# Kernel optimization log

Measured on AMD Instinct MI355X. Metric: run time of the kernel, lower is better.

The kernel has to match this reference:

```python
import jax, jax.numpy as jnp
import numpy as np

D_IN, D_OUT, N_EXP, D_HID = 1024, 1024, 8, 2048
N_TOK = 4096


def setup_inputs() -> dict:
    key = jax.random.key(0)
    ks = jax.random.split(key, 8)
    s_in = 1.0 / np.sqrt(D_IN)
    s_hid = 1.0 / np.sqrt(D_HID)
    s_out = 1.0 / np.sqrt(D_OUT)
    return {
        "x": jax.random.normal(ks[0], (N_TOK, D_IN), dtype=jnp.float32),
        # per-expert MLP weights, stacked along expert axis
        "W1": jax.random.uniform(ks[1], (N_EXP, D_IN, D_HID), jnp.float32, -s_in, s_in),
        "b1": jax.random.uniform(ks[2], (N_EXP, D_HID), jnp.float32, -s_in, s_in),
        "W2": jax.random.uniform(ks[3], (N_EXP, D_HID, D_OUT), jnp.float32, -s_hid, s_hid),
        "b2": jax.random.uniform(ks[4], (N_EXP, D_OUT), jnp.float32, -s_hid, s_hid),
        # shared final linear
        "Wf": jax.random.uniform(ks[5], (D_OUT, D_OUT), jnp.float32, -s_out, s_out),
        "bf": jax.random.uniform(ks[6], (D_OUT,), jnp.float32, -s_out, s_out),
    }


def reference(x, W1, b1, W2, b2, Wf, bf):
    # All experts applied to the same x: batched (grouped) GEMMs via einsum.
    h = jax.nn.relu(jnp.einsum("nd,edh->neh", x, W1) + b1[None])     # [N, E, H]
    y = jnp.einsum("neh,eho->neo", h, W2) + b2[None]                  # [N, E, O]
    z = jnp.einsum("neo,op->nep", y, Wf) + bf                         # shared final linear
    out = jnp.mean(z, axis=1)                                         # mean over experts
    return (out, 0)
```

## Files before the change

### kernel.cpp

```cpp
#include <hip/hip_runtime.h>
#include <hip/hip_bf16.h>


#define D_IN  1024
#define D_HID 2048
#define D_OUT 1024
#define N_EXP 8
#define N_TOK 4096

typedef __attribute__((ext_vector_type(4))) float  f32x4;
typedef __attribute__((ext_vector_type(8))) short  s16x8;
typedef __attribute__((ext_vector_type(4))) short  s16x4;
typedef __attribute__((ext_vector_type(8))) __bf16 b16x8;

static __device__ __forceinline__ f32x4 mfma16x16x32(s16x8 a, s16x8 b, f32x4 c) {
  return __builtin_amdgcn_mfma_f32_16x16x32_bf16(
      __builtin_bit_cast(b16x8, a), __builtin_bit_cast(b16x8, b), c, 0, 0, 0);
}

#define GLDS16(gptr, lptr)                                                         \
  __builtin_amdgcn_global_load_lds(                                               \
      (const __attribute__((address_space(1))) void*)(gptr),                      \
      (__attribute__((address_space(3))) void*)(lptr), 16, 0, 0)

#define WAITV(n) asm volatile("s_waitcnt vmcnt(" #n ")" ::: "memory")
#define SBAR()                                                                     \
  do {                                                                             \
    __builtin_amdgcn_sched_barrier(0);                                             \
    __builtin_amdgcn_s_barrier();                                                  \
    __builtin_amdgcn_sched_barrier(0);                                             \
  } while (0)

static __device__ __forceinline__ short f2b(float f) {
  return __builtin_bit_cast(short, __float2bfloat16(f));
}
static __device__ __forceinline__ float b2f(short s) {
  return __bfloat162float(__builtin_bit_cast(__hip_bfloat16, s));
}


__global__ void cast_x_kernel(const float* __restrict__ in, short* __restrict__ out, int n4) {
  int i = blockIdx.x * blockDim.x + threadIdx.x;
  if (i >= n4) return;
  f32x4 v = ((const f32x4*)in)[i];
  s16x4 o;
  o[0] = f2b(v[0]); o[1] = f2b(v[1]); o[2] = f2b(v[2]); o[3] = f2b(v[3]);
  ((s16x4*)out)[i] = o;
}

__global__ void tcast_kernel(const float* __restrict__ in, short* __restrict__ out, int R, int C) {
  __shared__ float t[32][33];
  size_t slab = (size_t)blockIdx.z * R * C;
  const float* src = in + slab;
  short* dst = out + slab;
  int c0 = blockIdx.x * 32, r0 = blockIdx.y * 32;
  int tx = threadIdx.x, ty = threadIdx.y;
#pragma unroll
  for (int i = 0; i < 32; i += 8)
    t[ty + i][tx] = src[(size_t)(r0 + ty + i) * C + c0 + tx];
  __syncthreads();
#pragma unroll
  for (int i = 0; i < 32; i += 8)
    dst[(size_t)(c0 + ty + i) * R + r0 + tx] = f2b(t[tx][ty + i]);
}

__global__ void b2mean_kernel(const float* __restrict__ b2, float* __restrict__ b2m) {
  int o = blockIdx.x * blockDim.x + threadIdx.x;
  if (o < D_OUT) {
    float s = 0.f;
#pragma unroll
    for (int e = 0; e < N_EXP; ++e) s += b2[e * D_OUT + o];
    b2m[o] = s * 0.125f;
  }
}


template <bool RELU>
__global__ __launch_bounds__(512, 2) void gemm256_p8_kernel(
    const short* __restrict__ A, const short* __restrict__ Bt,
    short* __restrict__ C, const float* __restrict__ bias,
    int K, int ldc, long sAe, long sBe, long sCe, long sBiasE) {
  extern __shared__ short lds[];
  const int tid = threadIdx.x, wid = tid >> 6, lane = tid & 63;
  const int e = blockIdx.z;
  const short* Ab = A + (size_t)e * sAe + (size_t)blockIdx.y * 256 * K;
  const short* Bb = Bt + (size_t)e * sBe + (size_t)blockIdx.x * 256 * K;

  const int strow = wid * 16 + (lane >> 2);
  const int stcol = ((lane & 3) ^ ((strow >> 1) & 3)) * 8;
  const int wm = wid >> 2, wn = wid & 3;
  const int lr = lane & 15;
  const int gp = ((lane >> 4) ^ ((lr >> 1) & 3)) * 8;

  f32x4 acc[8][4] = {};
  const int nkt = K / 64;
  const int niter = nkt / 2;

  auto SLOT = [&](int t, int ks, int ab) -> short* {
    return lds + (size_t)(t & 1) * 32768 + ab * 16384 + ks * 8192;
  };
  auto STAGE = [&](int t, int ks, int ab) {
    const short* src = ab ? Bb : Ab;
    short* dst = SLOT(t, ks, ab) + wid * 512;
    const size_t ko = (size_t)t * 64 + ks * 32 + stcol;
    GLDS16(src + (size_t)strow * K + ko, dst);
    GLDS16(src + (size_t)(128 + strow) * K + ko, dst + 4096);
  };
  auto LDA = [&](s16x8* av, int t, int h, int ks) {
    const short* s = SLOT(t, ks, 0);
#pragma unroll
    for (int m = 0; m < 4; ++m)
      av[m] = *(const s16x8*)&s[(wm * 128 + h * 64 + m * 16 + lr) * 32 + gp];
  };
  auto LDB = [&](s16x8* bv, int t, int ks) {
    const short* s = SLOT(t, ks, 1);
#pragma unroll
    for (int n = 0; n < 4; ++n)
      bv[n] = *(const s16x8*)&s[(wn * 64 + n * 16 + lr) * 32 + gp];
  };
  auto QUAD = [&](int h, const s16x8* av, const s16x8* bv) {
    __builtin_amdgcn_s_setprio(1);
#pragma unroll
    for (int m = 0; m < 4; ++m)
#pragma unroll
      for (int n = 0; n < 4; ++n)
        acc[h * 4 + m][n] = mfma16x16x32(av[m], bv[n], acc[h * 4 + m][n]);
    __builtin_amdgcn_s_setprio(0);
  };

  s16x8 av0[4], av1[4], bv0[4], bv1[4];

  STAGE(0, 0, 0); STAGE(0, 0, 1); STAGE(0, 1, 0); STAGE(0, 1, 1);
  STAGE(1, 0, 0); STAGE(1, 0, 1); STAGE(1, 1, 0);
  WAITV(10);
  SBAR();
  LDA(av1, 0, 0, 0);
  LDB(bv0, 0, 0);

  for (int i = 0; i < niter - 1; ++i) {
    const int t0 = 2 * i, t1 = t0 + 1;
     STAGE(t1, 1, 1); LDA(av0, t0, 1, 0);
           SBAR(); QUAD(0, av1, bv0);
     WAITV(8); STAGE(t0 + 2, 0, 0); LDA(av1, t0, 0, 1); LDB(bv1, t0, 1);
           SBAR(); QUAD(1, av0, bv0);
     STAGE(t0 + 2, 0, 1); LDA(av0, t0, 1, 1);
           SBAR(); QUAD(0, av1, bv1);
     WAITV(8); STAGE(t0 + 2, 1, 0); LDA(av1, t1, 0, 0); LDB(bv0, t1, 0);
           SBAR(); QUAD(1, av0, bv1);
     STAGE(t0 + 2, 1, 1); LDA(av0, t1, 1, 0);
           SBAR(); QUAD(0, av1, bv0);
     WAITV(8); STAGE(t0 + 3, 0, 0); LDA(av1, t1, 0, 1); LDB(bv1, t1, 1);
           SBAR(); QUAD(1, av0, bv0);
     STAGE(t0 + 3, 0, 1); LDA(av0, t1, 1, 1);
           SBAR(); QUAD(0, av1, bv1);
     WAITV(8); STAGE(t0 + 3, 1, 0); LDA(av1, t0 + 2, 0, 0); LDB(bv0, t0 + 2, 0);
           SBAR(); QUAD(1, av0, bv1);
  }
  {
    const int t0 = nkt - 2, t1 = nkt - 1;
     STAGE(t1, 1, 1); LDA(av0, t0, 1, 0);
           SBAR(); QUAD(0, av1, bv0);
     WAITV(8); LDA(av1, t0, 0, 1); LDB(bv1, t0, 1);
           SBAR(); QUAD(1, av0, bv0);
     LDA(av0, t0, 1, 1);
           SBAR(); QUAD(0, av1, bv1);
     WAITV(0); LDA(av1, t1, 0, 0); LDB(bv0, t1, 0);
           SBAR(); QUAD(1, av0, bv1);
     LDA(av0, t1, 1, 0);
           SBAR(); QUAD(0, av1, bv0);
     LDA(av1, t1, 0, 1); LDB(bv1, t1, 1);
           SBAR(); QUAD(1, av0, bv0);
     LDA(av0, t1, 1, 1);
           SBAR(); QUAD(0, av1, bv1);
     SBAR(); QUAD(1, av0, bv1);
  }

  __syncthreads();
  const int crow0 = wm * 128 + (lane >> 4) * 4;
  const int ccol0 = wn * 64 + lr;
#pragma unroll
  for (int ni = 0; ni < 4; ++ni) {
    const int col = ccol0 + ni * 16;
    const float bvv =
        bias ? bias[(size_t)e * sBiasE + (size_t)blockIdx.x * 256 + col] : 0.f;
#pragma unroll
    for (int mi = 0; mi < 8; ++mi)
#pragma unroll
      for (int j = 0; j < 4; ++j) {
        float v = acc[mi][ni][j] + bvv;
        if (RELU) v = v > 0.f ? v : 0.f;
        lds[(crow0 + mi * 16 + j) * 256 + col] = f2b(v);
      }
  }
  __syncthreads();
  short* Cp = C + (size_t)e * sCe + (size_t)blockIdx.y * 256 * ldc +
              (size_t)blockIdx.x * 256;
  const int cr = tid >> 5, cc = (tid & 31) * 8;
#pragma unroll
  for (int r = 0; r < 256; r += 16) {
    s16x8 v = *(const s16x8*)&lds[(r + cr) * 256 + cc];
    *(s16x8*)&Cp[(size_t)(r + cr) * ldc + cc] = v;
  }
}


template <bool RELU, bool OUTBF16>
__global__ __launch_bounds__(256) void gemm_bt_kernel(
    const short* __restrict__ A, const short* __restrict__ Bt, void* __restrict__ C,
    const float* __restrict__ bias, int K, int ldc,
    long sAe, long sBe, long sCe, long sBiasE) {
  constexpr int BM = 128, BN = 128, BK = 32;
  __shared__ short As[BM * BK];
  __shared__ short Bs[BN * BK];
  const int tid  = threadIdx.x;
  const int wid  = tid >> 6;
  const int lane = tid & 63;
  const int e    = blockIdx.z;

  const short* Ap = A + (size_t)e * sAe + (size_t)blockIdx.y * BM * K;
  const short* Bp = Bt + (size_t)e * sBe + (size_t)blockIdx.x * BN * K;

  const int srow = wid * 16 + (lane >> 2);
  const int scol = (lane & 3) * 8;
  const int wm = (wid >> 1) * 64, wn = (wid & 1) * 64;
  const int lr = lane & 15, lk = (lane >> 4) * 8;

  f32x4 acc[4][4] = {};
  const int nkt = K / BK;
  for (int kt = 0; kt < nkt; ++kt) {
    __syncthreads();
    const size_t ko = (size_t)kt * BK;
    GLDS16(Ap + (size_t)srow * K + ko + scol,        &As[wid * 512]);
    GLDS16(Ap + (size_t)(srow + 64) * K + ko + scol, &As[2048 + wid * 512]);
    GLDS16(Bp + (size_t)srow * K + ko + scol,        &Bs[wid * 512]);
    GLDS16(Bp + (size_t)(srow + 64) * K + ko + scol, &Bs[2048 + wid * 512]);
    __syncthreads();

    s16x8 a[4], b[4];
#pragma unroll
    for (int mi = 0; mi < 4; ++mi)
      a[mi] = *(const s16x8*)&As[(wm + mi * 16 + lr) * BK + lk];
#pragma unroll
    for (int ni = 0; ni < 4; ++ni)
      b[ni] = *(const s16x8*)&Bs[(wn + ni * 16 + lr) * BK + lk];
#pragma unroll
    for (int mi = 0; mi < 4; ++mi)
#pragma unroll
      for (int ni = 0; ni < 4; ++ni)
        acc[mi][ni] = mfma16x16x32(a[mi], b[ni], acc[mi][ni]);
  }

  const size_t Cbase = (size_t)e * sCe;
  const int row0 = blockIdx.y * BM + wm + (lane >> 4) * 4;
  const int col0 = blockIdx.x * BN + wn + lr;
#pragma unroll
  for (int ni = 0; ni < 4; ++ni) {
    const int col = col0 + ni * 16;
    const float bv = bias ? bias[(size_t)e * sBiasE + col] : 0.f;
#pragma unroll
    for (int mi = 0; mi < 4; ++mi) {
#pragma unroll
      for (int j = 0; j < 4; ++j) {
        float v = acc[mi][ni][j] + bv;
        if (RELU) v = v > 0.f ? v : 0.f;
        const size_t idx = Cbase + (size_t)(row0 + mi * 16 + j) * ldc + col;
        if (OUTBF16) ((short*)C)[idx] = f2b(v);
        else         ((float*)C)[idx] = v;
      }
    }
  }
}


__global__ void reduce_y_kernel(const short* __restrict__ yal, const float* __restrict__ b2m,
                                short* __restrict__ ybar, long slab, long total) {
  const size_t base = ((size_t)blockIdx.x * blockDim.x + threadIdx.x) * 8;
  if (base >= (size_t)total) return;
  float s[8] = {};
#pragma unroll
  for (int e = 0; e < N_EXP; ++e) {
    s16x8 v = *(const s16x8*)&yal[(size_t)e * slab + base];
#pragma unroll
    for (int j = 0; j < 8; ++j) s[j] += b2f(v[j]);
  }
  const int col = (int)(base & (D_OUT - 1));
  s16x8 o;
#pragma unroll
  for (int j = 0; j < 8; ++j) o[j] = f2b(s[j] * 0.125f + b2m[col + j]);
  *(s16x8*)&ybar[base] = o;
}

__global__ void tail_kernel(float* __restrict__ out, int from, int n) {
  int i = from + blockIdx.x * blockDim.x + threadIdx.x;
  if (i < n) out[i] = 0.f;
}


extern "C" void kernel_launch(void* const* d_in, const int* in_sizes, int n_in,
                              void* d_out, int out_size, void* d_ws, size_t ws_size,
                              hipStream_t stream) {
  const float* x  = (const float*)d_in[0];
  const float* W1 = (const float*)d_in[1];
  const float* b1 = (const float*)d_in[2];
  const float* W2 = (const float*)d_in[3];
  const float* b2 = (const float*)d_in[4];
  const float* Wf = (const float*)d_in[5];
  const float* bf = (const float*)d_in[6];
  float* out = (float*)d_out;

  const size_t sz_xb  = (size_t)N_TOK * D_IN * 2;
  const size_t sz_W1t = (size_t)N_EXP * D_HID * D_IN * 2;
  const size_t sz_W2t = (size_t)N_EXP * D_OUT * D_HID * 2;
  const size_t sz_Wft = (size_t)D_OUT * D_OUT * 2;
  const size_t sz_b2m = (size_t)D_OUT * 4;
  const size_t sz_ybr = (size_t)N_TOK * D_OUT * 2;
  const size_t fixed  = sz_xb + sz_W1t + sz_W2t + sz_Wft + sz_b2m + sz_ybr;
  const size_t per_full = (size_t)N_EXP * N_TOK * D_HID * 2
                        + (size_t)N_EXP * N_TOK * D_OUT * 2;
  int NC = 16;
  for (int c = 1; c <= 8; c <<= 1) {
    if (fixed + per_full / c <= ws_size) { NC = c; break; }
  }
  const int ntokc = N_TOK / NC;

  char* ws = (char*)d_ws;
  short* xb  = (short*)ws; ws += sz_xb;
  short* W1t = (short*)ws; ws += sz_W1t;
  short* W2t = (short*)ws; ws += sz_W2t;
  short* Wft = (short*)ws; ws += sz_Wft;
  float* b2m = (float*)ws; ws += sz_b2m;
  short* ybr = (short*)ws; ws += sz_ybr;
  short* h   = (short*)ws; ws += (size_t)N_EXP * ntokc * D_HID * 2;
  short* yal = (short*)ws;

  hipLaunchKernelGGL(cast_x_kernel, dim3(N_TOK * D_IN / 4 / 256), dim3(256), 0, stream,
                     x, xb, N_TOK * D_IN / 4);
  hipLaunchKernelGGL(tcast_kernel, dim3(D_HID / 32, D_IN / 32, N_EXP), dim3(32, 8), 0, stream,
                     W1, W1t, D_IN, D_HID);
  hipLaunchKernelGGL(tcast_kernel, dim3(D_OUT / 32, D_HID / 32, N_EXP), dim3(32, 8), 0, stream,
                     W2, W2t, D_HID, D_OUT);
  hipLaunchKernelGGL(tcast_kernel, dim3(D_OUT / 32, D_OUT / 32, 1), dim3(32, 8), 0, stream,
                     Wf, Wft, D_OUT, D_OUT);
  hipLaunchKernelGGL(b2mean_kernel, dim3(4), dim3(256), 0, stream, b2, b2m);

  const size_t ldsz = 131072;

  for (int c = 0; c < NC; ++c) {
    const short* xc = xb + (size_t)c * ntokc * D_IN;
    short* ybc = ybr + (size_t)c * ntokc * D_OUT;

    hipLaunchKernelGGL((gemm256_p8_kernel<true>),
                       dim3(D_HID / 256, ntokc / 256, N_EXP), dim3(512), ldsz, stream,
                       xc, W1t, h, b1, D_IN, D_HID,
                       0L, (long)D_HID * D_IN, (long)ntokc * D_HID, (long)D_HID);

    hipLaunchKernelGGL((gemm256_p8_kernel<false>),
                       dim3(D_OUT / 256, ntokc / 256, N_EXP), dim3(512), ldsz, stream,
                       h, W2t, yal, (const float*)nullptr, D_HID, D_OUT,
                       (long)ntokc * D_HID, (long)D_OUT * D_HID, (long)ntokc * D_OUT, 0L);

    hipLaunchKernelGGL(reduce_y_kernel, dim3(ntokc * D_OUT / 8 / 256), dim3(256), 0, stream,
                       yal, b2m, ybc, (long)ntokc * D_OUT, (long)ntokc * D_OUT);
  }

  hipLaunchKernelGGL((gemm_bt_kernel<false, false>),
                     dim3(D_OUT / 128, N_TOK / 128, 1), dim3(256), 0, stream,
                     ybr, Wft, d_out, bf, D_OUT, D_OUT, 0L, 0L, 0L, 0L);

  int tail = out_size - N_TOK * D_OUT;
  if (tail > 0)
    hipLaunchKernelGGL(tail_kernel, dim3((tail + 63) / 64), dim3(64), 0, stream,
                       out, N_TOK * D_OUT, out_size);
}
```

Measured before the change: 366.2 us.

## Restructure GEMM main loop to single-buffered register fragments with extra barriers

Rewrites the software-pipelined k-loop of the grouped GEMM kernel. Fragments are now loaded into a single register set right before use, gated by an explicit lgkmcnt(0) wait and an extra barrier per phase, instead of ping-ponging two fragment buffers so LDS reads overlap the previous MFMA quad. The global-to-LDS staging order and vmcnt thresholds are also changed. This frees registers, which may help occupancy, but it gives up LDS-read/MFMA overlap and doubles the barrier count.

```diff
diff --git a/kernel.cpp b/kernel.cpp
--- a/kernel.cpp
+++ b/kernel.cpp
@@ -28,6 +28,11 @@
   do {                                                                             \
     __builtin_amdgcn_sched_barrier(0);                                             \
     __builtin_amdgcn_s_barrier();                                                  \
+    __builtin_amdgcn_sched_barrier(0);                                             \
+  } while (0)
+#define LGKM0()                                                                    \
+  do {                                                                             \
+    asm volatile("s_waitcnt lgkmcnt(0)" ::: "memory");                             \
     __builtin_amdgcn_sched_barrier(0);                                             \
   } while (0)
 
@@ -128,51 +133,50 @@
     __builtin_amdgcn_s_setprio(0);
   };
 
-  s16x8 av0[4], av1[4], bv0[4], bv1[4];
-
-  STAGE(0, 0, 0); STAGE(0, 0, 1); STAGE(0, 1, 0); STAGE(0, 1, 1);
-  STAGE(1, 0, 0); STAGE(1, 0, 1); STAGE(1, 1, 0);
+  s16x8 av[4], bv[4];
+
+  STAGE(0, 0, 1); STAGE(0, 0, 0); STAGE(0, 1, 1); STAGE(0, 1, 0);
+  STAGE(1, 0, 1); STAGE(1, 0, 0); STAGE(1, 1, 1);
   WAITV(10);
   SBAR();
-  LDA(av1, 0, 0, 0);
-  LDB(bv0, 0, 0);
 
   for (int i = 0; i < niter - 1; ++i) {
-    const int t0 = 2 * i, t1 = t0 + 1;
-     STAGE(t1, 1, 1); LDA(av0, t0, 1, 0);
-           SBAR(); QUAD(0, av1, bv0);
-     WAITV(8); STAGE(t0 + 2, 0, 0); LDA(av1, t0, 0, 1); LDB(bv1, t0, 1);
-           SBAR(); QUAD(1, av0, bv0);
-     STAGE(t0 + 2, 0, 1); LDA(av0, t0, 1, 1);
-           SBAR(); QUAD(0, av1, bv1);
-     WAITV(8); STAGE(t0 + 2, 1, 0); LDA(av1, t1, 0, 0); LDB(bv0, t1, 0);
-           SBAR(); QUAD(1, av0, bv1);
-     STAGE(t0 + 2, 1, 1); LDA(av0, t1, 1, 0);
-           SBAR(); QUAD(0, av1, bv0);
-     WAITV(8); STAGE(t0 + 3, 0, 0); LDA(av1, t1, 0, 1); LDB(bv1, t1, 1);
-           SBAR(); QUAD(1, av0, bv0);
-     STAGE(t0 + 3, 0, 1); LDA(av0, t1, 1, 1);
-           SBAR(); QUAD(0, av1, bv1);
-     WAITV(8); STAGE(t0 + 3, 1, 0); LDA(av1, t0 + 2, 0, 0); LDB(bv0, t0 + 2, 0);
-           SBAR(); QUAD(1, av0, bv1);
+    const int t0 = 2 * i, t1 = t0 + 1, T2 = t0 + 2, T3 = t0 + 3;
+     LDA(av, t0, 0, 0); LDB(bv, t0, 0); STAGE(t1, 1, 0);
+           SBAR(); LGKM0(); QUAD(0, av, bv); SBAR();
+     LDA(av, t0, 1, 0); STAGE(T2, 0, 1);
+           SBAR(); LGKM0(); QUAD(1, av, bv); WAITV(10); SBAR();
+     LDA(av, t0, 0, 1); LDB(bv, t0, 1); STAGE(T2, 0, 0);
+           SBAR(); LGKM0(); QUAD(0, av, bv); SBAR();
+     LDA(av, t0, 1, 1); STAGE(T2, 1, 1);
+           SBAR(); LGKM0(); QUAD(1, av, bv); WAITV(10); SBAR();
+     LDA(av, t1, 0, 0); LDB(bv, t1, 0); STAGE(T2, 1, 0);
+           SBAR(); LGKM0(); QUAD(0, av, bv); SBAR();
+     LDA(av, t1, 1, 0); STAGE(T3, 0, 1);
+           SBAR(); LGKM0(); QUAD(1, av, bv); WAITV(10); SBAR();
+     LDA(av, t1, 0, 1); LDB(bv, t1, 1); STAGE(T3, 0, 0);
+           SBAR(); LGKM0(); QUAD(0, av, bv); SBAR();
+     LDA(av, t1, 1, 1); STAGE(T3, 1, 1);
+           SBAR(); LGKM0(); QUAD(1, av, bv); WAITV(10); SBAR();
   }
   {
     const int t0 = nkt - 2, t1 = nkt - 1;
-     STAGE(t1, 1, 1); LDA(av0, t0, 1, 0);
-           SBAR(); QUAD(0, av1, bv0);
-     WAITV(8); LDA(av1, t0, 0, 1); LDB(bv1, t0, 1);
-           SBAR(); QUAD(1, av0, bv0);
-     LDA(av0, t0, 1, 1);
-           SBAR(); QUAD(0, av1, bv1);
-     WAITV(0); LDA(av1, t1, 0, 0); LDB(bv0, t1, 0);
-           SBAR(); QUAD(1, av0, bv1);
-     LDA(av0, t1, 1, 0);
-           SBAR(); QUAD(0, av1, bv0);
-     LDA(av1, t1, 0, 1); LDB(bv1, t1, 1);
-           SBAR(); QUAD(1, av0, bv0);
-     LDA(av0, t1, 1, 1);
-           SBAR(); QUAD(0, av1, bv1);
-     SBAR(); QUAD(1, av0, bv1);
+     LDA(av, t0, 0, 0); LDB(bv, t0, 0); STAGE(t1, 1, 0);
+           SBAR(); LGKM0(); QUAD(0, av, bv); SBAR();
+     LDA(av, t0, 1, 0);
+           SBAR(); LGKM0(); QUAD(1, av, bv); WAITV(8); SBAR();
+     LDA(av, t0, 0, 1); LDB(bv, t0, 1);
+           SBAR(); LGKM0(); QUAD(0, av, bv); SBAR();
+     LDA(av, t0, 1, 1);
+           SBAR(); LGKM0(); QUAD(1, av, bv); WAITV(4); SBAR();
+     LDA(av, t1, 0, 0); LDB(bv, t1, 0);
+           SBAR(); LGKM0(); QUAD(0, av, bv); SBAR();
+     LDA(av, t1, 1, 0);
+           SBAR(); LGKM0(); QUAD(1, av, bv); WAITV(0); SBAR();
+     LDA(av, t1, 0, 1); LDB(bv, t1, 1);
+           SBAR(); LGKM0(); QUAD(0, av, bv); SBAR();
+     LDA(av, t1, 1, 1);
+           SBAR(); LGKM0(); QUAD(1, av, bv); SBAR();
   }
 
   __syncthreads();
```

After: 374.3 us. 1.02x slower.

## Load A operand directly from global into registers in first expert GEMM

Applied to the files above, without the earlier changes.

Adds a GEMM variant where only the B (weight) tile is staged through LDS via async global-to-LDS loads, while the A (token) fragments are loaded straight from global memory into registers in a double-buffered schedule interleaved with the MFMA quads. It is used for the first expert GEMM, where A is shared across all experts and column blocks. The goal is to halve LDS traffic and staging instructions. The cost is exposed global load latency on A, more vector registers, and uncoalesced 16-byte loads.

```diff
diff --git a/kernel.cpp b/kernel.cpp
--- a/kernel.cpp
+++ b/kernel.cpp
@@ -71,6 +71,122 @@
 #pragma unroll
     for (int e = 0; e < N_EXP; ++e) s += b2[e * D_OUT + o];
     b2m[o] = s * 0.125f;
+  }
+}
+
+
+template <bool RELU>
+__global__ __launch_bounds__(512, 2) void gemm256_areg_kernel(
+    const short* __restrict__ A, const short* __restrict__ Bt,
+    short* __restrict__ C, const float* __restrict__ bias,
+    int K, int ldc, long sAe, long sBe, long sCe, long sBiasE) {
+  extern __shared__ short lds[];
+  const int tid = threadIdx.x, wid = tid >> 6, lane = tid & 63;
+  const int e = blockIdx.z;
+  const short* Ab = A + (size_t)e * sAe + (size_t)blockIdx.y * 256 * K;
+  const short* Bb = Bt + (size_t)e * sBe + (size_t)blockIdx.x * 256 * K;
+
+  const int strow = wid * 16 + (lane >> 2);
+  const int stcol = ((lane & 3) ^ ((strow >> 1) & 3)) * 8;
+  const int wm = wid >> 2, wn = wid & 3;
+  const int lr = lane & 15;
+  const int gp = ((lane >> 4) ^ ((lr >> 1) & 3)) * 8;
+  const int kg = (lane >> 4) * 8;
+
+  f32x4 acc[8][4] = {};
+  const int nkt = K / 64;
+
+  auto BSLOT = [&](int t, int ks) -> short* {
+    return lds + (size_t)(t & 1) * 16384 + ks * 8192;
+  };
+  auto STAGEB = [&](int t, int ks) {
+    short* dst = BSLOT(t, ks) + wid * 512;
+    const size_t ko = (size_t)t * 64 + ks * 32 + stcol;
+    GLDS16(Bb + (size_t)strow * K + ko, dst);
+    GLDS16(Bb + (size_t)(128 + strow) * K + ko, dst + 4096);
+  };
+  auto LDB_ = [&](s16x8* bv, int t, int ks) {
+    const short* s = BSLOT(t, ks);
+#pragma unroll
+    for (int n = 0; n < 4; ++n)
+      bv[n] = *(const s16x8*)&s[(wn * 64 + n * 16 + lr) * 32 + gp];
+  };
+  auto LDAG = [&](s16x8* av, int t, int ks, int h) {
+    const short* base = Ab + (size_t)(wm * 128 + h * 64 + lr) * K +
+                        (size_t)t * 64 + ks * 32 + kg;
+#pragma unroll
+    for (int m = 0; m < 4; ++m)
+      av[m] = *(const s16x8*)(base + (size_t)m * 16 * K);
+  };
+  auto QUAD = [&](int h, const s16x8* av, const s16x8* bv) {
+    __builtin_amdgcn_s_setprio(1);
+#pragma unroll
+    for (int m = 0; m < 4; ++m)
+#pragma unroll
+      for (int n = 0; n < 4; ++n)
+        acc[h * 4 + m][n] = mfma16x16x32(av[m], bv[n], acc[h * 4 + m][n]);
+    __builtin_amdgcn_s_setprio(0);
+  };
+
+  s16x8 avX[4], avY[4], bv0[4], bv1[4];
+
+  STAGEB(0, 0); STAGEB(0, 1); STAGEB(1, 0); STAGEB(1, 1);
+  WAITV(0);
+  SBAR();
+  LDAG(avX, 0, 0, 0);
+  LDAG(avY, 0, 0, 1);
+  LDB_(bv0, 0, 0);
+
+  for (int t = 0; t < nkt - 2; ++t) {
+     WAITV(28); STAGEB(t + 2, 0); SBAR();
+           QUAD(0, avX, bv0); LDAG(avX, t, 1, 0);
+     LDB_(bv1, t, 1); SBAR();
+           QUAD(1, avY, bv0); LDAG(avY, t, 1, 1);
+     WAITV(24); STAGEB(t + 2, 1); SBAR();
+           QUAD(0, avX, bv1); LDAG(avX, t + 1, 0, 0);
+     LDB_(bv0, t + 1, 0); SBAR();
+           QUAD(1, avY, bv1); LDAG(avY, t + 1, 0, 1);
+  }
+  {
+    const int t = nkt - 2;
+     WAITV(28); SBAR(); QUAD(0, avX, bv0); LDAG(avX, t, 1, 0);
+     LDB_(bv1, t, 1); SBAR(); QUAD(1, avY, bv0); LDAG(avY, t, 1, 1);
+     WAITV(22); SBAR(); QUAD(0, avX, bv1); LDAG(avX, t + 1, 0, 0);
+     LDB_(bv0, t + 1, 0); SBAR(); QUAD(1, avY, bv1); LDAG(avY, t + 1, 0, 1);
+  }
+  {
+    const int t = nkt - 1;
+     WAITV(24); SBAR(); QUAD(0, avX, bv0); LDAG(avX, t, 1, 0);
+     LDB_(bv1, t, 1); SBAR(); QUAD(1, avY, bv0); LDAG(avY, t, 1, 1);
+     SBAR(); QUAD(0, avX, bv1);
+     SBAR(); QUAD(1, avY, bv1);
+  }
+
+  __syncthreads();
+  const int crow0 = wm * 128 + (lane >> 4) * 4;
+  const int ccol0 = wn * 64 + lr;
+#pragma unroll
+  for (int ni = 0; ni < 4; ++ni) {
+    const int col = ccol0 + ni * 16;
+    const float bvv =
+        bias ? bias[(size_t)e * sBiasE + (size_t)blockIdx.x * 256 + col] : 0.f;
+#pragma unroll
+    for (int mi = 0; mi < 8; ++mi)
+#pragma unroll
+      for (int j = 0; j < 4; ++j) {
+        float v = acc[mi][ni][j] + bvv;
+        if (RELU) v = v > 0.f ? v : 0.f;
+        lds[(crow0 + mi * 16 + j) * 256 + col] = f2b(v);
+      }
+  }
+  __syncthreads();
+  short* Cp = C + (size_t)e * sCe + (size_t)blockIdx.y * 256 * ldc +
+              (size_t)blockIdx.x * 256;
+  const int cr = tid >> 5, cc = (tid & 31) * 8;
+#pragma unroll
+  for (int r = 0; r < 256; r += 16) {
+    s16x8 v = *(const s16x8*)&lds[(r + cr) * 256 + cc];
+    *(s16x8*)&Cp[(size_t)(r + cr) * ldc + cc] = v;
   }
 }
 
@@ -349,7 +465,7 @@
     const short* xc = xb + (size_t)c * ntokc * D_IN;
     short* ybc = ybr + (size_t)c * ntokc * D_OUT;
 
-    hipLaunchKernelGGL((gemm256_p8_kernel<true>),
+    hipLaunchKernelGGL((gemm256_areg_kernel<true>),
                        dim3(D_HID / 256, ntokc / 256, N_EXP), dim3(512), ldsz, stream,
                        xc, W1t, h, b1, D_IN, D_HID,
                        0L, (long)D_HID * D_IN, (long)ntokc * D_HID, (long)D_HID);
```

Result: slower. 501.9 us (+37.1%).
